# Performance work log

Measured on AMD Instinct MI355X. Metric: run time of the kernel, lower is better.

## Reference

```python
import jax, jax.numpy as jnp
import numpy as np

TAU_PRE = 2.0
TAU_POST = 2.0
KH, KW = 3, 3
B, CIN, H, W = 16, 64, 66, 66
COUT = 128
HOUT, WOUT = H - KH + 1, W - KW + 1  # stride 1, padding 0


def setup_inputs() -> dict:
    key = jax.random.key(0)
    k1, k2, k3, k4, k5 = jax.random.split(key, 5)
    in_spike = jax.random.uniform(k1, (B, CIN, H, W), dtype=jnp.float32)
    out_spike = jax.random.uniform(k2, (B, COUT, HOUT, WOUT), dtype=jnp.float32)
    trace_pre = jax.random.uniform(k3, (B, CIN, H, W), dtype=jnp.float32)
    trace_post = jax.random.uniform(k4, (B, COUT, HOUT, WOUT), dtype=jnp.float32)
    weight = jax.random.normal(k5, (COUT, CIN, KH, KW), dtype=jnp.float32) * 0.05
    return {"in_spike": in_spike, "out_spike": out_spike,
            "trace_pre": trace_pre, "trace_post": trace_post, "weight": weight}


def reference(in_spike, out_spike, trace_pre, trace_post, weight):
    # Trace decay + spike accumulation (faithful to torch: tr - tr/tau + spike)
    tr_pre = trace_pre - trace_pre / TAU_PRE + in_spike    # [B,Cin,H,W]
    tr_post = trace_post - trace_post / TAU_POST + out_spike  # [B,Cout,Hout,Wout]

    rows = []
    for h in range(KH):
        cols = []
        for w in range(KW):
            pre = in_spike[:, :, h:h + HOUT, w:w + WOUT]   # [B,Cin,Hout,Wout]
            trp = tr_pre[:, :, h:h + HOUT, w:w + WOUT]     # [B,Cin,Hout,Wout]
            wk = weight[:, :, h, w]                        # [Cout,Cin]
            # sum over batch and spatial dims of outer products
            s_pre = jnp.einsum('bopq,bipq->oi', tr_post, pre)      # [Cout,Cin]
            s_post = jnp.einsum('bipq,bopq->oi', trp, out_spike)   # [Cout,Cin]
            cols.append(-wk * s_pre + wk * s_post)
        rows.append(jnp.stack(cols, axis=-1))  # [Cout,Cin,KW]
    delta_w = jnp.stack(rows, axis=-2)          # [Cout,Cin,KH,KW]
    return tr_pre, tr_post, delta_w
```

## Files before the change

### kernel.cpp

```cpp
#include <hip/hip_runtime.h>


typedef unsigned short ushort_t;
typedef unsigned int uint_t;
typedef __attribute__((ext_vector_type(8))) short short8;
typedef __attribute__((ext_vector_type(4))) float floatx4;
typedef __attribute__((ext_vector_type(2))) float floatx2;
typedef __attribute__((ext_vector_type(4))) int intx4;
typedef __attribute__((ext_vector_type(4))) uint_t uintx4;

#define N_POST   8388608
#define N_DW     73728
#define O_TRPOST 4460544
#define O_DW     12849152

#define MFMA_BLOCKS  384
#define FILLA_BLOCKS 1024
#define FILLB_BLOCKS 768
#define TOTAL_BLOCKS 2176
#define B_ROWS_PER_WAVE 22

__device__ __forceinline__ uint_t cvt2bf(float lo, float hi) {
  uint_t r; asm("v_cvt_pk_bf16_f32 %0, %1, %2" : "=v"(r) : "v"(lo), "v"(hi)); return r;
}
__device__ __forceinline__ uint_t cvt2bfn(float lo, float hi) {
  uint_t r; asm("v_cvt_pk_bf16_f32 %0, -%1, -%2" : "=v"(r) : "v"(lo), "v"(hi)); return r;
}
__device__ __forceinline__ int bsh2(int hi, int lo) {
  return (int)((((unsigned long long)(uint_t)hi << 32) | (uint_t)lo) >> 16);
}

__global__ __launch_bounds__(256, 2)
void k_main(const float* __restrict__ in_sp, const float* __restrict__ out_sp,
            const float* __restrict__ tpre, const float* __restrict__ tpost,
            float* __restrict__ o_trpre, float* __restrict__ o_trpost,
            float* __restrict__ partials, int use_ws) {
  const int bx0 = blockIdx.x;
  const int t = threadIdx.x;

  if (bx0 >= MFMA_BLOCKS) {
    if (bx0 < MFMA_BLOCKS + FILLA_BLOCKS) {
      int i4 = (bx0 - MFMA_BLOCKS) * 256 + t;
      #pragma unroll
      for (int it = 0; it < 8; ++it, i4 += FILLA_BLOCKS * 256) {
        floatx4 o = *(const floatx4*)(out_sp + i4 * 4);
        floatx4 p = *(const floatx4*)(tpost + i4 * 4);
        *(floatx4*)(o_trpost + i4 * 4) = 0.5f * p + o;
      }
    } else {
      const int l = t & 63;
      if (l >= 33) return;
      const int wid = (bx0 - (MFMA_BLOCKS + FILLA_BLOCKS)) * 4 + (t >> 6);
      #pragma unroll 2
      for (int it = 0; it < B_ROWS_PER_WAVE; ++it) {
        const int g = (wid * B_ROWS_PER_WAVE + it) * 66 + l * 2;
        floatx2 a = *(const floatx2*)(tpre + g);
        floatx2 c = *(const floatx2*)(in_sp + g);
        floatx2 v = { 0.5f * a.x + c.x, 0.5f * a.y + c.y };
        *(floatx2*)(o_trpre + g) = v;
      }
    }
    return;
  }
  if (!use_ws) return;

  __shared__ short LB[2][9728];
  const int kh = bx0 >> 7, bx = bx0 & 127;
  const int b = bx >> 3, p0 = (bx & 7) * 8;
  const int w = t >> 6, l = t & 63;
  const int quad = l >> 4, l16 = l & 15;
  const int si = t >> 2, sg = t & 3;

  const float* arow0 = out_sp + ((b * 128 + w * 32 + l16) * 4096 + quad * 8 + p0 * 64);
  const float* arow1 = tpost  + ((b * 128 + w * 32 + l16) * 4096 + quad * 8 + p0 * 64);
  const float* brow0 = tpre  + ((b * 64 + si) * 66 * 66 + sg * 16);
  const float* brow1 = in_sp + ((b * 64 + si) * 66 * 66 + sg * 16);
  short* Lrow = &LB[0][0] + si * 152 + sg * 16;

  floatx4 acc[3][2][4] = {};

  auto stageB = [&](int h, int buf) {
    const float* r0 = brow0 + h * 66;
    const float* r1 = brow1 + h * 66;
    floatx2 v0[8], v1[8];
    #pragma unroll
    for (int k = 0; k < 8; ++k) {
      v0[k] = *(const floatx2*)(r0 + 2 * k);
      v1[k] = *(const floatx2*)(r1 + 2 * k);
    }
    uintx4 u0a = { cvt2bf(v0[0].x, v0[0].y), cvt2bf(v0[1].x, v0[1].y),
                   cvt2bf(v0[2].x, v0[2].y), cvt2bf(v0[3].x, v0[3].y) };
    uintx4 u0b = { cvt2bf(v0[4].x, v0[4].y), cvt2bf(v0[5].x, v0[5].y),
                   cvt2bf(v0[6].x, v0[6].y), cvt2bf(v0[7].x, v0[7].y) };
    uintx4 u1a = { cvt2bf(v1[0].x, v1[0].y), cvt2bf(v1[1].x, v1[1].y),
                   cvt2bf(v1[2].x, v1[2].y), cvt2bf(v1[3].x, v1[3].y) };
    uintx4 u1b = { cvt2bf(v1[4].x, v1[4].y), cvt2bf(v1[5].x, v1[5].y),
                   cvt2bf(v1[6].x, v1[6].y), cvt2bf(v1[7].x, v1[7].y) };
    short* Lb = Lrow + buf * 9728;
    *(uintx4*)(Lb)      = u0a;
    *(uintx4*)(Lb + 8)  = u0b;
    *(uintx4*)(Lb + 72) = u1a;
    *(uintx4*)(Lb + 80) = u1b;
    if (sg == 3) {
      floatx2 t0 = *(const floatx2*)(r0 + 16);
      floatx2 t1 = *(const floatx2*)(r1 + 16);
      *(uint_t*)(Lb + 16) = cvt2bf(t0.x, t0.y);
      *(uint_t*)(Lb + 88) = cvt2bf(t1.x, t1.y);
    }
  };

  stageB(p0 + kh, 0);
  __syncthreads();

  for (int rr = 0; rr < 8; ++rr) {
    floatx4 ar[2][2][2][2];
    #pragma unroll
    for (int mt = 0; mt < 2; ++mt)
      #pragma unroll
      for (int ks = 0; ks < 2; ++ks)
        #pragma unroll
        for (int hf = 0; hf < 2; ++hf) {
          const int off = rr * 64 + mt * 65536 + ks * 32 + hf * 4;
          ar[0][mt][ks][hf] = *(const floatx4*)(arow0 + off);
          ar[1][mt][ks][hf] = *(const floatx4*)(arow1 + off);
        }
    if (rr < 7) stageB(p0 + rr + 1 + kh, (rr + 1) & 1);

    const short* Lbb = &LB[0][0] + (rr & 1) * 9728;
    #pragma unroll
    for (int ks = 0; ks < 2; ++ks) {
      short8 fa[2][2];
      #pragma unroll
      for (int mt = 0; mt < 2; ++mt) {
        uintx4 ua = { cvt2bf (ar[0][mt][ks][0].x, ar[0][mt][ks][0].y),
                      cvt2bf (ar[0][mt][ks][0].z, ar[0][mt][ks][0].w),
                      cvt2bf (ar[0][mt][ks][1].x, ar[0][mt][ks][1].y),
                      cvt2bf (ar[0][mt][ks][1].z, ar[0][mt][ks][1].w) };
        uintx4 un = { cvt2bfn(ar[1][mt][ks][0].x, ar[1][mt][ks][0].y),
                      cvt2bfn(ar[1][mt][ks][0].z, ar[1][mt][ks][0].w),
                      cvt2bfn(ar[1][mt][ks][1].x, ar[1][mt][ks][1].y),
                      cvt2bfn(ar[1][mt][ks][1].z, ar[1][mt][ks][1].w) };
        fa[0][mt] = __builtin_bit_cast(short8, ua);
        fa[1][mt] = __builtin_bit_cast(short8, un);
      }
      #pragma unroll
      for (int nt = 0; nt < 4; ++nt) {
        const int i = nt * 16 + l16;
        short8 fb[2][3];
        #pragma unroll
        for (int mat = 0; mat < 2; ++mat) {
          const int base = i * 152 + mat * 72 + ks * 32 + quad * 8;
          intx4 W = *(const intx4*)&Lbb[base];
          int W4 = *(const int*)&Lbb[base + 8];
          intx4 f0 = { W.x, W.y, W.z, W.w };
          intx4 f1 = { bsh2(W.y, W.x), bsh2(W.z, W.y), bsh2(W.w, W.z), bsh2(W4, W.w) };
          intx4 f2 = { W.y, W.z, W.w, W4 };
          fb[mat][0] = __builtin_bit_cast(short8, f0);
          fb[mat][1] = __builtin_bit_cast(short8, f1);
          fb[mat][2] = __builtin_bit_cast(short8, f2);
        }
        #pragma unroll
        for (int kw = 0; kw < 3; ++kw)
          #pragma unroll
          for (int mt = 0; mt < 2; ++mt) {
            acc[kw][mt][nt] = __builtin_amdgcn_mfma_f32_16x16x32_bf16(fa[0][mt], fb[0][kw], acc[kw][mt][nt], 0, 0, 0);
            acc[kw][mt][nt] = __builtin_amdgcn_mfma_f32_16x16x32_bf16(fa[1][mt], fb[1][kw], acc[kw][mt][nt], 0, 0, 0);
          }
      }
    }
    __syncthreads();
  }

  #pragma unroll
  for (int kw = 0; kw < 3; ++kw) {
    float* slice = partials + (size_t)((kh * 3 + kw) * 128 + bx) * 8192;
    #pragma unroll
    for (int mt = 0; mt < 2; ++mt)
      #pragma unroll
      for (int nt = 0; nt < 4; ++nt)
        #pragma unroll
        for (int rg = 0; rg < 4; ++rg) {
          const int o = w * 32 + mt * 16 + quad * 4 + rg;
          const int i = nt * 16 + l16;
          slice[o * 64 + i] = acc[kw][mt][nt][rg];
        }
  }
}

__global__ void k_finalize(const float* __restrict__ partials,
                           const float* __restrict__ weight, float* __restrict__ dw) {
  int tid = blockIdx.x * 256 + threadIdx.x;
  int e = tid >> 13, oi = tid & 8191;
  float s = 0.f;
  #pragma unroll 8
  for (int c = 0; c < 128; ++c) s += partials[(size_t)(e * 128 + c) * 8192 + oi];
  int o = oi >> 6, i = oi & 63;
  int wi = (o * 64 + i) * 9 + e;
  dw[wi] = 0.5f * weight[wi] * s;
}

__global__ void k_naive(const float* __restrict__ out_sp, const float* __restrict__ tpost,
                        const float* __restrict__ tpre, const float* __restrict__ in_sp,
                        const float* __restrict__ weight, float* __restrict__ dw) {
  int tid = blockIdx.x * 256 + threadIdx.x;
  int e = tid >> 13, oi = tid & 8191;
  int o = oi >> 6, i = oi & 63;
  int kh = e / 3, kw = e - kh * 3;
  float acc = 0.f;
  for (int b = 0; b < 16; ++b)
    for (int p = 0; p < 64; ++p) {
      const float* ga = out_sp + ((b * 128 + o) * 64 + p) * 64;
      const float* gn = tpost + ((b * 128 + o) * 64 + p) * 64;
      const float* gb = tpre + ((b * 64 + i) * 66 + p + kh) * 66 + kw;
      const float* gm = in_sp + ((b * 64 + i) * 66 + p + kh) * 66 + kw;
      for (int q = 0; q < 64; ++q) acc += ga[q] * gb[q] - gn[q] * gm[q];
    }
  int wi = (o * 64 + i) * 9 + kh * 3 + kw;
  dw[wi] = 0.5f * weight[wi] * acc;
}

extern "C" void kernel_launch(void* const* d_in, const int* in_sizes, int n_in,
                              void* d_out, int out_size, void* d_ws, size_t ws_size,
                              hipStream_t stream) {
  const float* in_sp  = (const float*)d_in[0];
  const float* out_sp = (const float*)d_in[1];
  const float* tpre   = (const float*)d_in[2];
  const float* tpost  = (const float*)d_in[3];
  const float* weight = (const float*)d_in[4];
  float* out = (float*)d_out;
  float* o_trpre  = out;
  float* o_trpost = out + O_TRPOST;
  float* o_dw     = out + O_DW;

  const size_t WS_NEED = (size_t)9 * 128 * 8192 * 4;
  const int use_mfma = (ws_size >= WS_NEED) ? 1 : 0;
  float* partials = (float*)d_ws;

  k_main<<<TOTAL_BLOCKS, 256, 0, stream>>>(in_sp, out_sp, tpre, tpost,
                                           o_trpre, o_trpost, partials, use_mfma);
  if (use_mfma) {
    k_finalize<<<N_DW / 256, 256, 0, stream>>>(partials, weight, o_dw);
  } else {
    k_naive<<<N_DW / 256, 256, 0, stream>>>(out_sp, tpost, tpre, in_sp, weight, o_dw);
  }
}
```

Measured before the change: 198.2 us.

## Load B operand fragments directly from global memory instead of LDS staging

Removes the double-buffered LDS staging of the pre-synaptic rows and the per-row __syncthreads. Each lane now loads its B fragment straight from global memory as float2 values, converts them to bf16 in registers and builds the shifted kw variants there. This drops LDS traffic and barriers, but each wave now issues its own redundant, less coalesced global loads (every wave reloads the same B data) and repeats the conversions per wave.

```diff
diff --git a/kernel.cpp b/kernel.cpp
--- a/kernel.cpp
+++ b/kernel.cpp
@@ -20,11 +20,11 @@
 #define TOTAL_BLOCKS 2176
 #define B_ROWS_PER_WAVE 22
 
-__device__ __forceinline__ uint_t cvt2bf(float lo, float hi) {
-  uint_t r; asm("v_cvt_pk_bf16_f32 %0, %1, %2" : "=v"(r) : "v"(lo), "v"(hi)); return r;
-}
-__device__ __forceinline__ uint_t cvt2bfn(float lo, float hi) {
-  uint_t r; asm("v_cvt_pk_bf16_f32 %0, -%1, -%2" : "=v"(r) : "v"(lo), "v"(hi)); return r;
+__device__ __forceinline__ int cvt2bf(float lo, float hi) {
+  int r; asm("v_cvt_pk_bf16_f32 %0, %1, %2" : "=v"(r) : "v"(lo), "v"(hi)); return r;
+}
+__device__ __forceinline__ int cvt2bfn(float lo, float hi) {
+  int r; asm("v_cvt_pk_bf16_f32 %0, -%1, -%2" : "=v"(r) : "v"(lo), "v"(hi)); return r;
 }
 __device__ __forceinline__ int bsh2(int hi, int lo) {
   return (int)((((unsigned long long)(uint_t)hi << 32) | (uint_t)lo) >> 16);
@@ -64,53 +64,17 @@
   }
   if (!use_ws) return;
 
-  __shared__ short LB[2][9728];
   const int kh = bx0 >> 7, bx = bx0 & 127;
   const int b = bx >> 3, p0 = (bx & 7) * 8;
   const int w = t >> 6, l = t & 63;
   const int quad = l >> 4, l16 = l & 15;
-  const int si = t >> 2, sg = t & 3;
 
   const float* arow0 = out_sp + ((b * 128 + w * 32 + l16) * 4096 + quad * 8 + p0 * 64);
   const float* arow1 = tpost  + ((b * 128 + w * 32 + l16) * 4096 + quad * 8 + p0 * 64);
-  const float* brow0 = tpre  + ((b * 64 + si) * 66 * 66 + sg * 16);
-  const float* brow1 = in_sp + ((b * 64 + si) * 66 * 66 + sg * 16);
-  short* Lrow = &LB[0][0] + si * 152 + sg * 16;
+  const float* bbase0 = tpre  + ((b * 64 + l16) * 4356 + (p0 + kh) * 66 + quad * 8);
+  const float* bbase1 = in_sp + ((b * 64 + l16) * 4356 + (p0 + kh) * 66 + quad * 8);
 
   floatx4 acc[3][2][4] = {};
-
-  auto stageB = [&](int h, int buf) {
-    const float* r0 = brow0 + h * 66;
-    const float* r1 = brow1 + h * 66;
-    floatx2 v0[8], v1[8];
-    #pragma unroll
-    for (int k = 0; k < 8; ++k) {
-      v0[k] = *(const floatx2*)(r0 + 2 * k);
-      v1[k] = *(const floatx2*)(r1 + 2 * k);
-    }
-    uintx4 u0a = { cvt2bf(v0[0].x, v0[0].y), cvt2bf(v0[1].x, v0[1].y),
-                   cvt2bf(v0[2].x, v0[2].y), cvt2bf(v0[3].x, v0[3].y) };
-    uintx4 u0b = { cvt2bf(v0[4].x, v0[4].y), cvt2bf(v0[5].x, v0[5].y),
-                   cvt2bf(v0[6].x, v0[6].y), cvt2bf(v0[7].x, v0[7].y) };
-    uintx4 u1a = { cvt2bf(v1[0].x, v1[0].y), cvt2bf(v1[1].x, v1[1].y),
-                   cvt2bf(v1[2].x, v1[2].y), cvt2bf(v1[3].x, v1[3].y) };
-    uintx4 u1b = { cvt2bf(v1[4].x, v1[4].y), cvt2bf(v1[5].x, v1[5].y),
-                   cvt2bf(v1[6].x, v1[6].y), cvt2bf(v1[7].x, v1[7].y) };
-    short* Lb = Lrow + buf * 9728;
-    *(uintx4*)(Lb)      = u0a;
-    *(uintx4*)(Lb + 8)  = u0b;
-    *(uintx4*)(Lb + 72) = u1a;
-    *(uintx4*)(Lb + 80) = u1b;
-    if (sg == 3) {
-      floatx2 t0 = *(const floatx2*)(r0 + 16);
-      floatx2 t1 = *(const floatx2*)(r1 + 16);
-      *(uint_t*)(Lb + 16) = cvt2bf(t0.x, t0.y);
-      *(uint_t*)(Lb + 88) = cvt2bf(t1.x, t1.y);
-    }
-  };
-
-  stageB(p0 + kh, 0);
-  __syncthreads();
 
   for (int rr = 0; rr < 8; ++rr) {
     floatx4 ar[2][2][2][2];
@@ -124,40 +88,56 @@
           ar[0][mt][ks][hf] = *(const floatx4*)(arow0 + off);
           ar[1][mt][ks][hf] = *(const floatx4*)(arow1 + off);
         }
-    if (rr < 7) stageB(p0 + rr + 1 + kh, (rr + 1) & 1);
-
-    const short* Lbb = &LB[0][0] + (rr & 1) * 9728;
+
     #pragma unroll
     for (int ks = 0; ks < 2; ++ks) {
       short8 fa[2][2];
       #pragma unroll
       for (int mt = 0; mt < 2; ++mt) {
-        uintx4 ua = { cvt2bf (ar[0][mt][ks][0].x, ar[0][mt][ks][0].y),
-                      cvt2bf (ar[0][mt][ks][0].z, ar[0][mt][ks][0].w),
-                      cvt2bf (ar[0][mt][ks][1].x, ar[0][mt][ks][1].y),
-                      cvt2bf (ar[0][mt][ks][1].z, ar[0][mt][ks][1].w) };
-        uintx4 un = { cvt2bfn(ar[1][mt][ks][0].x, ar[1][mt][ks][0].y),
-                      cvt2bfn(ar[1][mt][ks][0].z, ar[1][mt][ks][0].w),
-                      cvt2bfn(ar[1][mt][ks][1].x, ar[1][mt][ks][1].y),
-                      cvt2bfn(ar[1][mt][ks][1].z, ar[1][mt][ks][1].w) };
+        uintx4 ua = { (uint_t)cvt2bf (ar[0][mt][ks][0].x, ar[0][mt][ks][0].y),
+                      (uint_t)cvt2bf (ar[0][mt][ks][0].z, ar[0][mt][ks][0].w),
+                      (uint_t)cvt2bf (ar[0][mt][ks][1].x, ar[0][mt][ks][1].y),
+                      (uint_t)cvt2bf (ar[0][mt][ks][1].z, ar[0][mt][ks][1].w) };
+        uintx4 un = { (uint_t)cvt2bfn(ar[1][mt][ks][0].x, ar[1][mt][ks][0].y),
+                      (uint_t)cvt2bfn(ar[1][mt][ks][0].z, ar[1][mt][ks][0].w),
+                      (uint_t)cvt2bfn(ar[1][mt][ks][1].x, ar[1][mt][ks][1].y),
+                      (uint_t)cvt2bfn(ar[1][mt][ks][1].z, ar[1][mt][ks][1].w) };
         fa[0][mt] = __builtin_bit_cast(short8, ua);
         fa[1][mt] = __builtin_bit_cast(short8, un);
       }
       #pragma unroll
       for (int nt = 0; nt < 4; ++nt) {
-        const int i = nt * 16 + l16;
+        const int boff = rr * 66 + nt * 69696 + ks * 32;
+        const float* r0 = bbase0 + boff;
+        const float* r1 = bbase1 + boff;
+        floatx2 q0[5], q1[5];
+        #pragma unroll
+        for (int k2 = 0; k2 < 5; ++k2) {
+          q0[k2] = *(const floatx2*)(r0 + 2 * k2);
+          q1[k2] = *(const floatx2*)(r1 + 2 * k2);
+        }
+        int c0[5], c1[5];
+        #pragma unroll
+        for (int k2 = 0; k2 < 5; ++k2) {
+          c0[k2] = cvt2bf(q0[k2].x, q0[k2].y);
+          c1[k2] = cvt2bf(q1[k2].x, q1[k2].y);
+        }
         short8 fb[2][3];
-        #pragma unroll
-        for (int mat = 0; mat < 2; ++mat) {
-          const int base = i * 152 + mat * 72 + ks * 32 + quad * 8;
-          intx4 W = *(const intx4*)&Lbb[base];
-          int W4 = *(const int*)&Lbb[base + 8];
-          intx4 f0 = { W.x, W.y, W.z, W.w };
-          intx4 f1 = { bsh2(W.y, W.x), bsh2(W.z, W.y), bsh2(W.w, W.z), bsh2(W4, W.w) };
-          intx4 f2 = { W.y, W.z, W.w, W4 };
-          fb[mat][0] = __builtin_bit_cast(short8, f0);
-          fb[mat][1] = __builtin_bit_cast(short8, f1);
-          fb[mat][2] = __builtin_bit_cast(short8, f2);
+        {
+          intx4 f00 = { c0[0], c0[1], c0[2], c0[3] };
+          intx4 f01 = { bsh2(c0[1], c0[0]), bsh2(c0[2], c0[1]),
+                        bsh2(c0[3], c0[2]), bsh2(c0[4], c0[3]) };
+          intx4 f02 = { c0[1], c0[2], c0[3], c0[4] };
+          intx4 f10 = { c1[0], c1[1], c1[2], c1[3] };
+          intx4 f11 = { bsh2(c1[1], c1[0]), bsh2(c1[2], c1[1]),
+                        bsh2(c1[3], c1[2]), bsh2(c1[4], c1[3]) };
+          intx4 f12 = { c1[1], c1[2], c1[3], c1[4] };
+          fb[0][0] = __builtin_bit_cast(short8, f00);
+          fb[0][1] = __builtin_bit_cast(short8, f01);
+          fb[0][2] = __builtin_bit_cast(short8, f02);
+          fb[1][0] = __builtin_bit_cast(short8, f10);
+          fb[1][1] = __builtin_bit_cast(short8, f11);
+          fb[1][2] = __builtin_bit_cast(short8, f12);
         }
         #pragma unroll
         for (int kw = 0; kw < 3; ++kw)
@@ -168,7 +148,6 @@
           }
       }
     }
-    __syncthreads();
   }
 
   #pragma unroll
```

Result: slower. 233.5 us (+17.8%).

## Repartition MFMA work: longer spatial reduction per block, split output channels

Applied to the files above, without the earlier changes.

Each MFMA block now covers half the output channels (64) over 32 spatial rows instead of all 128 channels over 8 rows. This cuts the partial-sum buffer from 128 to 32 slices per kernel tap, which shrinks partial writes and the finalize reduction, and it halves the MFMA block count. In exchange the B tile is staged and converted twice (once per channel half), per-wave MFMA work per staged row drops, and there are fewer blocks available to fill the GPU.

```diff
diff --git a/kernel.cpp b/kernel.cpp
--- a/kernel.cpp
+++ b/kernel.cpp
@@ -14,17 +14,18 @@
 #define O_TRPOST 4460544
 #define O_DW     12849152
 
-#define MFMA_BLOCKS  384
+#define MFMA_BLOCKS  192
 #define FILLA_BLOCKS 1024
 #define FILLB_BLOCKS 768
-#define TOTAL_BLOCKS 2176
+#define TOTAL_BLOCKS 1984
 #define B_ROWS_PER_WAVE 22
-
-__device__ __forceinline__ uint_t cvt2bf(float lo, float hi) {
-  uint_t r; asm("v_cvt_pk_bf16_f32 %0, %1, %2" : "=v"(r) : "v"(lo), "v"(hi)); return r;
-}
-__device__ __forceinline__ uint_t cvt2bfn(float lo, float hi) {
-  uint_t r; asm("v_cvt_pk_bf16_f32 %0, -%1, -%2" : "=v"(r) : "v"(lo), "v"(hi)); return r;
+#define NSPLIT 32
+
+__device__ __forceinline__ int cvt2bf(float lo, float hi) {
+  int r; asm("v_cvt_pk_bf16_f32 %0, %1, %2" : "=v"(r) : "v"(lo), "v"(hi)); return r;
+}
+__device__ __forceinline__ int cvt2bfn(float lo, float hi) {
+  int r; asm("v_cvt_pk_bf16_f32 %0, -%1, -%2" : "=v"(r) : "v"(lo), "v"(hi)); return r;
 }
 __device__ __forceinline__ int bsh2(int hi, int lo) {
   return (int)((((unsigned long long)(uint_t)hi << 32) | (uint_t)lo) >> 16);
@@ -65,19 +66,20 @@
   if (!use_ws) return;
 
   __shared__ short LB[2][9728];
-  const int kh = bx0 >> 7, bx = bx0 & 127;
-  const int b = bx >> 3, p0 = (bx & 7) * 8;
+  const int kh = bx0 >> 6, r = bx0 & 63;
+  const int b = r >> 2, half = (r >> 1) & 1, pc = r & 1;
+  const int p0 = pc * 32;
   const int w = t >> 6, l = t & 63;
   const int quad = l >> 4, l16 = l & 15;
   const int si = t >> 2, sg = t & 3;
 
-  const float* arow0 = out_sp + ((b * 128 + w * 32 + l16) * 4096 + quad * 8 + p0 * 64);
-  const float* arow1 = tpost  + ((b * 128 + w * 32 + l16) * 4096 + quad * 8 + p0 * 64);
-  const float* brow0 = tpre  + ((b * 64 + si) * 66 * 66 + sg * 16);
-  const float* brow1 = in_sp + ((b * 64 + si) * 66 * 66 + sg * 16);
+  const float* arow0 = out_sp + ((b * 128 + half * 64 + w * 16 + l16) * 4096 + quad * 8 + p0 * 64);
+  const float* arow1 = tpost  + ((b * 128 + half * 64 + w * 16 + l16) * 4096 + quad * 8 + p0 * 64);
+  const float* brow0 = tpre  + ((b * 64 + si) * 4356 + sg * 16);
+  const float* brow1 = in_sp + ((b * 64 + si) * 4356 + sg * 16);
   short* Lrow = &LB[0][0] + si * 152 + sg * 16;
 
-  floatx4 acc[3][2][4] = {};
+  floatx4 acc[3][4] = {};
 
   auto stageB = [&](int h, int buf) {
     const float* r0 = brow0 + h * 66;
@@ -88,14 +90,14 @@
       v0[k] = *(const floatx2*)(r0 + 2 * k);
       v1[k] = *(const floatx2*)(r1 + 2 * k);
     }
-    uintx4 u0a = { cvt2bf(v0[0].x, v0[0].y), cvt2bf(v0[1].x, v0[1].y),
-                   cvt2bf(v0[2].x, v0[2].y), cvt2bf(v0[3].x, v0[3].y) };
-    uintx4 u0b = { cvt2bf(v0[4].x, v0[4].y), cvt2bf(v0[5].x, v0[5].y),
-                   cvt2bf(v0[6].x, v0[6].y), cvt2bf(v0[7].x, v0[7].y) };
-    uintx4 u1a = { cvt2bf(v1[0].x, v1[0].y), cvt2bf(v1[1].x, v1[1].y),
-                   cvt2bf(v1[2].x, v1[2].y), cvt2bf(v1[3].x, v1[3].y) };
-    uintx4 u1b = { cvt2bf(v1[4].x, v1[4].y), cvt2bf(v1[5].x, v1[5].y),
-                   cvt2bf(v1[6].x, v1[6].y), cvt2bf(v1[7].x, v1[7].y) };
+    uintx4 u0a = { (uint_t)cvt2bf(v0[0].x, v0[0].y), (uint_t)cvt2bf(v0[1].x, v0[1].y),
+                   (uint_t)cvt2bf(v0[2].x, v0[2].y), (uint_t)cvt2bf(v0[3].x, v0[3].y) };
+    uintx4 u0b = { (uint_t)cvt2bf(v0[4].x, v0[4].y), (uint_t)cvt2bf(v0[5].x, v0[5].y),
+                   (uint_t)cvt2bf(v0[6].x, v0[6].y), (uint_t)cvt2bf(v0[7].x, v0[7].y) };
+    uintx4 u1a = { (uint_t)cvt2bf(v1[0].x, v1[0].y), (uint_t)cvt2bf(v1[1].x, v1[1].y),
+                   (uint_t)cvt2bf(v1[2].x, v1[2].y), (uint_t)cvt2bf(v1[3].x, v1[3].y) };
+    uintx4 u1b = { (uint_t)cvt2bf(v1[4].x, v1[4].y), (uint_t)cvt2bf(v1[5].x, v1[5].y),
+                   (uint_t)cvt2bf(v1[6].x, v1[6].y), (uint_t)cvt2bf(v1[7].x, v1[7].y) };
     short* Lb = Lrow + buf * 9728;
     *(uintx4*)(Lb)      = u0a;
     *(uintx4*)(Lb + 8)  = u0b;
@@ -104,44 +106,41 @@
     if (sg == 3) {
       floatx2 t0 = *(const floatx2*)(r0 + 16);
       floatx2 t1 = *(const floatx2*)(r1 + 16);
-      *(uint_t*)(Lb + 16) = cvt2bf(t0.x, t0.y);
-      *(uint_t*)(Lb + 88) = cvt2bf(t1.x, t1.y);
+      *(uint_t*)(Lb + 16) = (uint_t)cvt2bf(t0.x, t0.y);
+      *(uint_t*)(Lb + 88) = (uint_t)cvt2bf(t1.x, t1.y);
     }
   };
 
   stageB(p0 + kh, 0);
   __syncthreads();
 
-  for (int rr = 0; rr < 8; ++rr) {
-    floatx4 ar[2][2][2][2];
-    #pragma unroll
-    for (int mt = 0; mt < 2; ++mt)
-      #pragma unroll
-      for (int ks = 0; ks < 2; ++ks)
-        #pragma unroll
-        for (int hf = 0; hf < 2; ++hf) {
-          const int off = rr * 64 + mt * 65536 + ks * 32 + hf * 4;
-          ar[0][mt][ks][hf] = *(const floatx4*)(arow0 + off);
-          ar[1][mt][ks][hf] = *(const floatx4*)(arow1 + off);
-        }
-    if (rr < 7) stageB(p0 + rr + 1 + kh, (rr + 1) & 1);
+  for (int rr = 0; rr < 32; ++rr) {
+    floatx4 ar[2][2][2];
+    #pragma unroll
+    for (int ks = 0; ks < 2; ++ks)
+      #pragma unroll
+      for (int hf = 0; hf < 2; ++hf) {
+        const int off = rr * 64 + ks * 32 + hf * 4;
+        ar[0][ks][hf] = *(const floatx4*)(arow0 + off);
+        ar[1][ks][hf] = *(const floatx4*)(arow1 + off);
+      }
+    if (rr < 31) stageB(p0 + rr + 1 + kh, (rr + 1) & 1);
 
     const short* Lbb = &LB[0][0] + (rr & 1) * 9728;
     #pragma unroll
     for (int ks = 0; ks < 2; ++ks) {
-      short8 fa[2][2];
-      #pragma unroll
-      for (int mt = 0; mt < 2; ++mt) {
-        uintx4 ua = { cvt2bf (ar[0][mt][ks][0].x, ar[0][mt][ks][0].y),
-                      cvt2bf (ar[0][mt][ks][0].z, ar[0][mt][ks][0].w),
-                      cvt2bf (ar[0][mt][ks][1].x, ar[0][mt][ks][1].y),
-                      cvt2bf (ar[0][mt][ks][1].z, ar[0][mt][ks][1].w) };
-        uintx4 un = { cvt2bfn(ar[1][mt][ks][0].x, ar[1][mt][ks][0].y),
-                      cvt2bfn(ar[1][mt][ks][0].z, ar[1][mt][ks][0].w),
-                      cvt2bfn(ar[1][mt][ks][1].x, ar[1][mt][ks][1].y),
-                      cvt2bfn(ar[1][mt][ks][1].z, ar[1][mt][ks][1].w) };
-        fa[0][mt] = __builtin_bit_cast(short8, ua);
-        fa[1][mt] = __builtin_bit_cast(short8, un);
+      short8 fa[2];
+      {
+        uintx4 ua = { (uint_t)cvt2bf (ar[0][ks][0].x, ar[0][ks][0].y),
+                      (uint_t)cvt2bf (ar[0][ks][0].z, ar[0][ks][0].w),
+                      (uint_t)cvt2bf (ar[0][ks][1].x, ar[0][ks][1].y),
+                      (uint_t)cvt2bf (ar[0][ks][1].z, ar[0][ks][1].w) };
+        uintx4 un = { (uint_t)cvt2bfn(ar[1][ks][0].x, ar[1][ks][0].y),
+                      (uint_t)cvt2bfn(ar[1][ks][0].z, ar[1][ks][0].w),
+                      (uint_t)cvt2bfn(ar[1][ks][1].x, ar[1][ks][1].y),
+                      (uint_t)cvt2bfn(ar[1][ks][1].z, ar[1][ks][1].w) };
+        fa[0] = __builtin_bit_cast(short8, ua);
+        fa[1] = __builtin_bit_cast(short8, un);
       }
       #pragma unroll
       for (int nt = 0; nt < 4; ++nt) {
@@ -160,12 +159,10 @@
           fb[mat][2] = __builtin_bit_cast(short8, f2);
         }
         #pragma unroll
-        for (int kw = 0; kw < 3; ++kw)
-          #pragma unroll
-          for (int mt = 0; mt < 2; ++mt) {
-            acc[kw][mt][nt] = __builtin_amdgcn_mfma_f32_16x16x32_bf16(fa[0][mt], fb[0][kw], acc[kw][mt][nt], 0, 0, 0);
-            acc[kw][mt][nt] = __builtin_amdgcn_mfma_f32_16x16x32_bf16(fa[1][mt], fb[1][kw], acc[kw][mt][nt], 0, 0, 0);
-          }
+        for (int kw = 0; kw < 3; ++kw) {
+          acc[kw][nt] = __builtin_amdgcn_mfma_f32_16x16x32_bf16(fa[0], fb[0][kw], acc[kw][nt], 0, 0, 0);
+          acc[kw][nt] = __builtin_amdgcn_mfma_f32_16x16x32_bf16(fa[1], fb[1][kw], acc[kw][nt], 0, 0, 0);
+        }
       }
     }
     __syncthreads();
@@ -173,17 +170,15 @@
 
   #pragma unroll
   for (int kw = 0; kw < 3; ++kw) {
-    float* slice = partials + (size_t)((kh * 3 + kw) * 128 + bx) * 8192;
-    #pragma unroll
-    for (int mt = 0; mt < 2; ++mt)
-      #pragma unroll
-      for (int nt = 0; nt < 4; ++nt)
-        #pragma unroll
-        for (int rg = 0; rg < 4; ++rg) {
-          const int o = w * 32 + mt * 16 + quad * 4 + rg;
-          const int i = nt * 16 + l16;
-          slice[o * 64 + i] = acc[kw][mt][nt][rg];
-        }
+    float* slice = partials + (size_t)((kh * 3 + kw) * NSPLIT + b * 2 + pc) * 8192;
+    #pragma unroll
+    for (int nt = 0; nt < 4; ++nt)
+      #pragma unroll
+      for (int rg = 0; rg < 4; ++rg) {
+        const int o = half * 64 + w * 16 + quad * 4 + rg;
+        const int i = nt * 16 + l16;
+        slice[o * 64 + i] = acc[kw][nt][rg];
+      }
   }
 }
 
@@ -193,7 +188,7 @@
   int e = tid >> 13, oi = tid & 8191;
   float s = 0.f;
   #pragma unroll 8
-  for (int c = 0; c < 128; ++c) s += partials[(size_t)(e * 128 + c) * 8192 + oi];
+  for (int c = 0; c < NSPLIT; ++c) s += partials[(size_t)(e * NSPLIT + c) * 8192 + oi];
   int o = oi >> 6, i = oi & 63;
   int wi = (o * 64 + i) * 9 + e;
   dw[wi] = 0.5f * weight[wi] * s;
@@ -232,7 +227,7 @@
   float* o_trpost = out + O_TRPOST;
   float* o_dw     = out + O_DW;
 
-  const size_t WS_NEED = (size_t)9 * 128 * 8192 * 4;
+  const size_t WS_NEED = (size_t)9 * NSPLIT * 8192 * 4;
   const int use_mfma = (ws_size >= WS_NEED) ? 1 : 0;
   float* partials = (float*)d_ws;
 
```

Result: slower. 238.1 us (+20.2%).
